# Kernel tuning notes

Hardware: AMD Instinct MI355X
Metric: run time of the kernel (lower is better)

## Reference

```python
import jax, jax.numpy as jnp
import numpy as np

LN_EPS = 1e-5

def _layernorm(x, w, b):
    mu = jnp.mean(x, axis=-1, keepdims=True)
    var = jnp.mean(jnp.square(x - mu), axis=-1, keepdims=True)
    return (x - mu) * jax.lax.rsqrt(var + LN_EPS) * w + b

def setup_inputs() -> dict:
    key = jax.random.key(0)
    ks = jax.random.split(key, 8)
    B, T, C, N = 4, 4096, 1024, 64
    H = 4 * C  # mlp hidden
    x = jax.random.normal(ks[0], (B, T, C), dtype=jnp.float32)
    log_tau = jnp.zeros((N,), dtype=jnp.float32)           # log(1.0)
    log_dt = jnp.zeros((), dtype=jnp.float32)              # log(1.0)
    mix = jax.random.normal(ks[1], (C, N), dtype=jnp.float32) * 0.02
    D = jnp.ones((C,), dtype=jnp.float32)
    norm1_w = jnp.ones((C,), dtype=jnp.float32)
    norm1_b = jnp.zeros((C,), dtype=jnp.float32)
    norm2_w = jnp.ones((C,), dtype=jnp.float32)
    norm2_b = jnp.zeros((C,), dtype=jnp.float32)
    fc1_w = jax.random.normal(ks[2], (H, C), dtype=jnp.float32) * 0.02
    fc1_b = jnp.zeros((H,), dtype=jnp.float32)
    fc2_w = jax.random.normal(ks[3], (C, H), dtype=jnp.float32) * 0.02
    fc2_b = jnp.zeros((C,), dtype=jnp.float32)
    return {"x": x, "log_tau": log_tau, "log_dt": log_dt, "mix": mix, "D": D,
            "norm1_w": norm1_w, "norm1_b": norm1_b, "norm2_w": norm2_w, "norm2_b": norm2_b,
            "fc1_w": fc1_w, "fc1_b": fc1_b, "fc2_w": fc2_w, "fc2_b": fc2_b}

def _s4d(u, log_tau, log_dt, mix, D):
    # u: (B, C, T). K_c[t] = sum_j mix[c,j] * exp(-softplus(log_tau[j])*softplus(log_dt)*t)
    B, C, T = u.shape
    tau = jax.nn.softplus(log_tau)                    # (N,)
    dt = jax.nn.softplus(log_dt)                      # scalar
    t = jnp.arange(T, dtype=jnp.float32)              # (T,)
    E = jnp.exp(-(tau * dt)[:, None] * t[None, :])    # (N, T)
    # torch module computes the exponent table under no_grad (cached buffer)
    E = jax.lax.stop_gradient(E)
    K = mix @ E                                       # (C, T)
    # causal depthwise conv via FFT: y[b,c,t] = sum_{s<=t} K[c,t-s] u[b,c,s]
    n = 2 * T
    Uf = jnp.fft.rfft(u, n=n, axis=-1)                # (B, C, n//2+1)
    Kf = jnp.fft.rfft(K, n=n, axis=-1)                # (C, n//2+1)
    y = jnp.fft.irfft(Uf * Kf[None], n=n, axis=-1)[..., :T]
    return y + D[None, :, None] * u

def reference(x, log_tau, log_dt, mix, D, norm1_w, norm1_b, norm2_w, norm2_b,
              fc1_w, fc1_b, fc2_w, fc2_b):
    # x: (B, T, C)
    h = _layernorm(x, norm1_w, norm1_b)
    h2 = _s4d(jnp.swapaxes(h, 1, 2), log_tau, log_dt, mix, D)  # (B, C, T)
    x = x + jnp.swapaxes(h2, 1, 2)                    # alpha_s4 = 1.0
    g = _layernorm(x, norm2_w, norm2_b)
    g = jax.nn.gelu(g @ fc1_w.T + fc1_b, approximate=False)
    g = g @ fc2_w.T + fc2_b
    return x + g                                      # alpha_mlp = 1.0
```

## Files before the change

kernel.cpp:

```cpp
#include <hip/hip_runtime.h>
#include <math.h>

typedef __attribute__((ext_vector_type(8))) short bf16x8;
typedef __attribute__((ext_vector_type(4))) float f32x4;

__device__ __forceinline__ unsigned short f2bf(float f) {
  union { float f; unsigned u; } v; v.f = f;
  unsigned r = v.u + 0x7fff + ((v.u >> 16) & 1);
  return (unsigned short)(r >> 16);
}

__device__ __forceinline__ float bf2f(unsigned short h) {
  union { unsigned u; float f; } v; v.u = ((unsigned)h) << 16;
  return v.f;
}

__device__ __forceinline__ void gll16(const void* g, void* l) {
  __builtin_amdgcn_global_load_lds(
      (const __attribute__((address_space(1))) void*)g,
      (__attribute__((address_space(3))) void*)l, 16, 0, 0);
}

#define BB 4
#define TT 4096
#define CC 1024
#define HH 4096
#define MM 16384

#define SWZ(row, byteoff) (((row) << 7) + ((byteoff) ^ (((row) & 7) << 4)))

__global__ __launch_bounds__(256) void ln_f32_kernel(
    const float* __restrict__ x, const float* __restrict__ w,
    const float* __restrict__ b, float* __restrict__ out)
{
  size_t row = blockIdx.x;
  const float4* xr = (const float4*)(x + row * CC);
  int tid = threadIdx.x;
  float4 v = xr[tid];
  float s = v.x + v.y + v.z + v.w;
  float sq = v.x*v.x + v.y*v.y + v.z*v.z + v.w*v.w;
  for (int o = 32; o; o >>= 1) { s += __shfl_xor(s, o); sq += __shfl_xor(sq, o); }
  __shared__ float ss[4], ssq[4];
  int wv = tid >> 6, lane = tid & 63;
  if (lane == 0) { ss[wv] = s; ssq[wv] = sq; }
  __syncthreads();
  s = ss[0] + ss[1] + ss[2] + ss[3];
  sq = ssq[0] + ssq[1] + ssq[2] + ssq[3];
  float mu = s * (1.f / CC);
  float var = sq * (1.f / CC) - mu * mu;
  float rstd = rsqrtf(var + 1e-5f);
  float4 wv4 = ((const float4*)w)[tid];
  float4 bv4 = ((const float4*)b)[tid];
  float4 o;
  o.x = (v.x - mu) * rstd * wv4.x + bv4.x;
  o.y = (v.y - mu) * rstd * wv4.y + bv4.y;
  o.z = (v.z - mu) * rstd * wv4.z + bv4.z;
  o.w = (v.w - mu) * rstd * wv4.w + bv4.w;
  ((float4*)(out + row * CC))[tid] = o;
}

__global__ __launch_bounds__(256) void ln_bf16_kernel(
    const float* __restrict__ x, const float* __restrict__ w,
    const float* __restrict__ b, unsigned short* __restrict__ out)
{
  size_t row = blockIdx.x;
  const float4* xr = (const float4*)(x + row * CC);
  int tid = threadIdx.x;
  float4 v = xr[tid];
  float s = v.x + v.y + v.z + v.w;
  float sq = v.x*v.x + v.y*v.y + v.z*v.z + v.w*v.w;
  for (int o = 32; o; o >>= 1) { s += __shfl_xor(s, o); sq += __shfl_xor(sq, o); }
  __shared__ float ss[4], ssq[4];
  int wv = tid >> 6, lane = tid & 63;
  if (lane == 0) { ss[wv] = s; ssq[wv] = sq; }
  __syncthreads();
  s = ss[0] + ss[1] + ss[2] + ss[3];
  sq = ssq[0] + ssq[1] + ssq[2] + ssq[3];
  float mu = s * (1.f / CC);
  float var = sq * (1.f / CC) - mu * mu;
  float rstd = rsqrtf(var + 1e-5f);
  float4 wv4 = ((const float4*)w)[tid];
  float4 bv4 = ((const float4*)b)[tid];
  ushort4 o;
  o.x = f2bf((v.x - mu) * rstd * wv4.x + bv4.x);
  o.y = f2bf((v.y - mu) * rstd * wv4.y + bv4.y);
  o.z = f2bf((v.z - mu) * rstd * wv4.z + bv4.z);
  o.w = f2bf((v.w - mu) * rstd * wv4.w + bv4.w);
  ((ushort4*)(out + row * CC))[tid] = o;
}

__global__ __launch_bounds__(256) void transpose_kernel(
    const float* __restrict__ in, float* __restrict__ out)
{
  __shared__ float tile[64][65];
  size_t boff = (size_t)blockIdx.z * TT * CC;
  int r0 = blockIdx.y * 64;
  int c0 = blockIdx.x * 64;
  int tid = threadIdx.x;
#pragma unroll
  for (int i = 0; i < 16; ++i) {
    int idx = tid + i * 256;
    int r = idx >> 6, cx = idx & 63;
    tile[r][cx] = in[boff + (size_t)(r0 + r) * CC + c0 + cx];
  }
  __syncthreads();
#pragma unroll
  for (int i = 0; i < 16; ++i) {
    int idx = tid + i * 256;
    int r = idx >> 6, cx = idx & 63;
    out[boff + (size_t)(c0 + r) * TT + r0 + cx] = tile[cx][r];
  }
}

__global__ __launch_bounds__(256) void transadd_kernel(
    const float* __restrict__ y, const float* __restrict__ x,
    float* __restrict__ x2)
{
  __shared__ float tile[64][65];
  size_t boff = (size_t)blockIdx.z * TT * CC;
  int t0 = blockIdx.x * 64;
  int c0 = blockIdx.y * 64;
  int tid = threadIdx.x;
#pragma unroll
  for (int i = 0; i < 16; ++i) {
    int idx = tid + i * 256;
    int r = idx >> 6, cx = idx & 63;
    tile[r][cx] = y[boff + (size_t)(c0 + r) * TT + t0 + cx];
  }
  __syncthreads();
#pragma unroll
  for (int i = 0; i < 16; ++i) {
    int idx = tid + i * 256;
    int r = idx >> 6, cx = idx & 63;
    size_t off = boff + (size_t)(t0 + r) * CC + c0 + cx;
    x2[off] = x[off] + tile[cx][r];
  }
}

__global__ __launch_bounds__(256) void s4d_kernel(
    const float* __restrict__ hT,
    const float* __restrict__ log_tau,
    const float* __restrict__ log_dt,
    const float* __restrict__ mix,
    const float* __restrict__ Dv,
    float* __restrict__ y)
{
  int bc = blockIdx.x;
  int c = bc & (CC - 1);
  int tid = threadIdx.x;
  int lane = tid & 63, w = tid >> 6;
  int m = lane & 15, g = lane >> 4;

  __shared__ unsigned short s_uh[64 * 64], s_ul[64 * 64];
  __shared__ unsigned short s_A2[64 * 64], s_Ac[64 * 64];
  __shared__ unsigned short s_T[64 * 64], s_Wt[64 * 64];
  __shared__ float s_P[64 * 64];
  __shared__ float s_a[64], s_rL[64], s_mix[64], s_K[64], s_Kp[4 * 64];

  const float4* urow = (const float4*)(hT + (size_t)bc * TT);
#pragma unroll
  for (int q = 0; q < 4; ++q) {
    int i = tid + q * 256;
    float4 v = urow[i];
    int row = i >> 4;
    int colb = (i & 15) * 8;
    float f[4] = {v.x, v.y, v.z, v.w};
    ushort4 hh, ll;
    unsigned short* hp = (unsigned short*)&hh;
    unsigned short* lp = (unsigned short*)&ll;
#pragma unroll
    for (int r = 0; r < 4; ++r) {
      unsigned short hb = f2bf(f[r]);
      hp[r] = hb;
      lp[r] = f2bf(f[r] - bf2f(hb));
    }
    *(ushort4*)((char*)s_uh + SWZ(row, colb)) = hh;
    *(ushort4*)((char*)s_ul + SWZ(row, colb)) = ll;
  }
  if (tid < 64) {
    float lt = log_tau[tid];
    float tau = (lt > 20.f) ? lt : log1pf(expf(lt));
    float ld = log_dt[0];
    float dt = (ld > 20.f) ? ld : log1pf(expf(ld));
    float a = tau * dt;
    s_a[tid] = a;
    s_rL[tid] = expf(-64.f * a);
    s_mix[tid] = mix[c * 64 + tid];
  }
  __syncthreads();

#pragma unroll
  for (int e = 0; e < 16; ++e) {
    int idx = tid + e * 256;
    int rA = idx >> 6, cA = idx & 63;
    s_A2[SWZ(rA, cA * 2) >> 1] = f2bf(expf(-s_a[rA] * (float)(63 - cA)));
    s_Ac[SWZ(rA, cA * 2) >> 1] = f2bf(expf(-s_a[cA] * (float)(rA + 1)));
  }
  __syncthreads();

  {
    int d = tid & 63, q = tid >> 6;
    float p = 0.f;
    if (d == 0) {
#pragma unroll
      for (int j = 16 * q; j < 16 * q + 16; ++j) p += s_mix[j];
    } else {
#pragma unroll
      for (int j = 16 * q; j < 16 * q + 16; ++j)
        p = fmaf(s_mix[j], bf2f(s_Ac[SWZ(d - 1, j * 2) >> 1]), p);
    }
    s_Kp[q * 64 + d] = p;
  }

  {
    f32x4 accP[4] = {};
    bf16x8 a2f[2];
#pragma unroll
    for (int ks = 0; ks < 2; ++ks)
      a2f[ks] = *(const bf16x8*)((const char*)s_A2 + SWZ(16 * w + m, ks * 64 + g * 16));
#pragma unroll
    for (int ct = 0; ct < 4; ++ct) {
#pragma unroll
      for (int ks = 0; ks < 2; ++ks) {
        bf16x8 bh = *(const bf16x8*)((const char*)s_uh + SWZ(ct * 16 + m, ks * 64 + g * 16));
        bf16x8 bl = *(const bf16x8*)((const char*)s_ul + SWZ(ct * 16 + m, ks * 64 + g * 16));
        accP[ct] = __builtin_amdgcn_mfma_f32_16x16x32_bf16(a2f[ks], bh, accP[ct], 0, 0, 0);
        accP[ct] = __builtin_amdgcn_mfma_f32_16x16x32_bf16(a2f[ks], bl, accP[ct], 0, 0, 0);
      }
    }
#pragma unroll
    for (int ct = 0; ct < 4; ++ct)
      *(f32x4*)&s_P[(ct * 16 + m) * 64 + 16 * w + g * 4] = accP[ct];
  }
  __syncthreads();

  if (tid < 64)
    s_K[tid] = s_Kp[tid] + s_Kp[64 + tid] + s_Kp[128 + tid] + s_Kp[192 + tid];
  __syncthreads();

#pragma unroll
  for (int e = 0; e < 16; ++e) {
    int idx = tid + e * 256;
    int t = idx >> 6, s = idx & 63;
    float val = (s <= t) ? s_K[t - s] : 0.f;
    s_T[SWZ(t, s * 2) >> 1] = f2bf(val);
  }
  if (tid < 64) {
    int j = tid;
    float S = 0.f, rL = s_rL[j], mj = s_mix[j];
    for (int k = 0; k < 64; ++k) {
      s_Wt[SWZ(k, j * 2) >> 1] = f2bf(mj * S);
      S = fmaf(rL, S, s_P[k * 64 + j]);
    }
  }
  __syncthreads();

  f32x4 accY[4] = {};
  {
    bf16x8 acf[2], tf[2];
#pragma unroll
    for (int ks = 0; ks < 2; ++ks) {
      acf[ks] = *(const bf16x8*)((const char*)s_Ac + SWZ(16 * w + m, ks * 64 + g * 16));
      tf[ks]  = *(const bf16x8*)((const char*)s_T  + SWZ(16 * w + m, ks * 64 + g * 16));
    }
#pragma unroll
    for (int ct = 0; ct < 4; ++ct) {
#pragma unroll
      for (int ks = 0; ks < 2; ++ks) {
        bf16x8 bw  = *(const bf16x8*)((const char*)s_Wt + SWZ(ct * 16 + m, ks * 64 + g * 16));
        bf16x8 uhf = *(const bf16x8*)((const char*)s_uh + SWZ(ct * 16 + m, ks * 64 + g * 16));
        bf16x8 ulf = *(const bf16x8*)((const char*)s_ul + SWZ(ct * 16 + m, ks * 64 + g * 16));
        accY[ct] = __builtin_amdgcn_mfma_f32_16x16x32_bf16(acf[ks], bw,  accY[ct], 0, 0, 0);
        accY[ct] = __builtin_amdgcn_mfma_f32_16x16x32_bf16(tf[ks],  uhf, accY[ct], 0, 0, 0);
        accY[ct] = __builtin_amdgcn_mfma_f32_16x16x32_bf16(tf[ks],  ulf, accY[ct], 0, 0, 0);
      }
    }
  }

  float Dc = Dv[c];
  float* yrow = y + (size_t)bc * TT;
#pragma unroll
  for (int ct = 0; ct < 4; ++ct) {
    int k = ct * 16 + m;
    int t0 = 16 * w + g * 4;
    float4 o;
    float* op = (float*)&o;
#pragma unroll
    for (int r = 0; r < 4; ++r) {
      int t = t0 + r;
      float uf = bf2f(s_uh[SWZ(k, t * 2) >> 1]) + bf2f(s_ul[SWZ(k, t * 2) >> 1]);
      op[r] = accY[ct][r] + Dc * uf;
    }
    *(float4*)(yrow + k * 64 + t0) = o;
  }
}

__global__ __launch_bounds__(256) void cvt_bf16_kernel(
    const float* __restrict__ in, unsigned short* __restrict__ out)
{
  int i = blockIdx.x * 256 + threadIdx.x;
  float4 v = ((const float4*)in)[i];
  ushort4 o;
  o.x = f2bf(v.x); o.y = f2bf(v.y); o.z = f2bf(v.z); o.w = f2bf(v.w);
  ((ushort4*)out)[i] = o;
}


#define GEMM256_BODY(A_, lda_, B_, ldb_, K_)                                   \
  __shared__ unsigned short sA[2][256 * 64];                                   \
  __shared__ unsigned short sB[2][256 * 64];                                   \
  int id = blockIdx.x;                                                         \
  int swz = (id & 7) * cpx + (id >> 3);                                        \
  int m0 = (swz / NB) * 256, n0 = (swz % NB) * 256;                            \
  int tid = threadIdx.x, lane = tid & 63;                                      \
  int wid = tid >> 6, wm = wid >> 2, wn = wid & 3;                             \
  int m = lane & 15, g = lane >> 4;                                            \
  const unsigned short* aSrc[4];                                               \
  const unsigned short* bSrc[4];                                               \
  int ldsOff[4];                                                               \
  _Pragma("unroll")                                                            \
  for (int i = 0; i < 4; ++i) {                                                \
    int j = i * 512 + tid;                                                     \
    int row = j >> 3;                                                          \
    int colb = ((j & 7) * 16) ^ ((row & 7) << 4);                              \
    aSrc[i] = (A_) + (size_t)(m0 + row) * (lda_) + (colb >> 1);                \
    bSrc[i] = (B_) + (size_t)(n0 + row) * (ldb_) + (colb >> 1);                \
    ldsOff[i] = j * 8;                                                         \
  }                                                                            \
  f32x4 acc[8][4] = {};                                                        \
  int nt = (K_) >> 6;                                                          \
                                                \
  _Pragma("unroll")                                                            \
  for (int i = 0; i < 4; ++i) gll16(aSrc[i], &sA[0][ldsOff[i]]);               \
  _Pragma("unroll")                                                            \
  for (int i = 0; i < 4; ++i) gll16(bSrc[i], &sB[0][ldsOff[i]]);               \
  _Pragma("unroll")                                                            \
  for (int i = 0; i < 4; ++i) gll16(aSrc[i] + 64, &sA[1][ldsOff[i]]);          \
  _Pragma("unroll")                                                            \
  for (int i = 0; i < 4; ++i) gll16(bSrc[i] + 64, &sB[1][ldsOff[i]]);          \
  asm volatile("s_waitcnt vmcnt(8)" ::: "memory");                             \
  asm volatile("s_barrier" ::: "memory");                                      \
  int cur = 0;                                                                 \
  for (int kt = 0; kt < nt; ++kt) {                                            \
    const unsigned short* sAc = sA[cur];                                       \
    const unsigned short* sBc = sB[cur];                                       \
    bf16x8 bfr[4][2];                                                          \
    _Pragma("unroll")                                                          \
    for (int ni = 0; ni < 4; ++ni)                                             \
      _Pragma("unroll")                                                        \
      for (int ks = 0; ks < 2; ++ks)                                           \
        bfr[ni][ks] = *(const bf16x8*)((const char*)sBc +                      \
                        SWZ(wn * 64 + ni * 16 + m, ks * 64 + g * 16));         \
    _Pragma("unroll")                                                          \
    for (int q = 0; q < 4; ++q) {                                              \
      bf16x8 af[2][2];                                                         \
      _Pragma("unroll")                                                        \
      for (int mi = 0; mi < 2; ++mi)                                           \
        _Pragma("unroll")                                                      \
        for (int ks = 0; ks < 2; ++ks)                                         \
          af[mi][ks] = *(const bf16x8*)((const char*)sAc +                     \
                         SWZ(wm * 128 + (q * 2 + mi) * 16 + m,                 \
                             ks * 64 + g * 16));                               \
      __builtin_amdgcn_s_setprio(1);                                           \
      _Pragma("unroll")                                                        \
      for (int mi = 0; mi < 2; ++mi)                                           \
        _Pragma("unroll")                                                      \
        for (int ni = 0; ni < 4; ++ni) {                                       \
          acc[q * 2 + mi][ni] = __builtin_amdgcn_mfma_f32_16x16x32_bf16(       \
              af[mi][0], bfr[ni][0], acc[q * 2 + mi][ni], 0, 0, 0);            \
          acc[q * 2 + mi][ni] = __builtin_amdgcn_mfma_f32_16x16x32_bf16(       \
              af[mi][1], bfr[ni][1], acc[q * 2 + mi][ni], 0, 0, 0);            \
        }                                                                      \
      __builtin_amdgcn_s_setprio(0);                                           \
    }                                                                          \
    if (kt + 1 < nt) {                                                         \
      asm volatile("s_barrier" ::: "memory");   \
      if (kt + 2 < nt) {                                                       \
        int ko = (kt + 2) << 6;                                                \
        _Pragma("unroll")                                                      \
        for (int i = 0; i < 4; ++i) gll16(aSrc[i] + ko, &sA[cur][ldsOff[i]]);  \
        _Pragma("unroll")                                                      \
        for (int i = 0; i < 4; ++i) gll16(bSrc[i] + ko, &sB[cur][ldsOff[i]]);  \
        asm volatile("s_waitcnt vmcnt(8)" ::: "memory");                       \
      } else {                                                                 \
        asm volatile("s_waitcnt vmcnt(0)" ::: "memory");                       \
      }                                                                        \
      asm volatile("s_barrier" ::: "memory");   \
      cur ^= 1;                                                                \
    }                                                                          \
  }

__global__ __launch_bounds__(512, 2) void gemm_gelu_kernel(
    const unsigned short* __restrict__ A, int lda,
    const unsigned short* __restrict__ Bw, int ldb,
    const float* __restrict__ bias, unsigned short* __restrict__ Out, int ldo,
    int K, int NB, int cpx)
{
  GEMM256_BODY(A, lda, Bw, ldb, K)

#pragma unroll
  for (int mi = 0; mi < 8; ++mi) {
    int row = m0 + wm * 128 + mi * 16 + g * 4;
#pragma unroll
    for (int ni = 0; ni < 4; ++ni) {
      int col = n0 + wn * 64 + ni * 16 + m;
      float bcol = bias[col];
#pragma unroll
      for (int r = 0; r < 4; ++r) {
        float v = acc[mi][ni][r] + bcol;
        v = 0.5f * v * (1.f + erff(v * 0.70710678118f));
        Out[(size_t)(row + r) * ldo + col] = f2bf(v);
      }
    }
  }
}

__global__ __launch_bounds__(512, 2) void gemm_acc_kernel(
    const unsigned short* __restrict__ A, int lda,
    const unsigned short* __restrict__ Bw, int ldb,
    const float* __restrict__ bias,
    const float* add, float* Out, int K, int NB, int cpx)
{
  GEMM256_BODY(A, lda, Bw, ldb, K)

#pragma unroll
  for (int mi = 0; mi < 8; ++mi) {
    int row = m0 + wm * 128 + mi * 16 + g * 4;
#pragma unroll
    for (int ni = 0; ni < 4; ++ni) {
      int col = n0 + wn * 64 + ni * 16 + m;
      float bcol = bias ? bias[col] : 0.f;
#pragma unroll
      for (int r = 0; r < 4; ++r) {
        size_t off = (size_t)(row + r) * CC + col;
        Out[off] = acc[mi][ni][r] + bcol + add[off];
      }
    }
  }
}

extern "C" void kernel_launch(void* const* d_in, const int* in_sizes, int n_in,
                              void* d_out, int out_size, void* d_ws, size_t ws_size,
                              hipStream_t stream)
{
  const float* x       = (const float*)d_in[0];
  const float* log_tau = (const float*)d_in[1];
  const float* log_dt  = (const float*)d_in[2];
  const float* mix     = (const float*)d_in[3];
  const float* Dv      = (const float*)d_in[4];
  const float* n1w     = (const float*)d_in[5];
  const float* n1b     = (const float*)d_in[6];
  const float* n2w     = (const float*)d_in[7];
  const float* n2b     = (const float*)d_in[8];
  const float* w1      = (const float*)d_in[9];
  const float* b1      = (const float*)d_in[10];
  const float* w2      = (const float*)d_in[11];
  const float* b2      = (const float*)d_in[12];

  char* ws = (char*)d_ws;
  float* buf0 = (float*)ws;
  float* buf1 = (float*)(ws + (64ull << 20));
  unsigned short* a2  = (unsigned short*)(ws + (128ull << 20));
  unsigned short* w1b = (unsigned short*)(ws + (160ull << 20));
  unsigned short* w2b = (unsigned short*)(ws + (168ull << 20));
  unsigned short* act = (unsigned short*)buf0;
  float* out = (float*)d_out;

  ln_f32_kernel<<<MM, 256, 0, stream>>>(x, n1w, n1b, buf0);
  transpose_kernel<<<dim3(CC / 64, TT / 64, BB), 256, 0, stream>>>(buf0, buf1);
  s4d_kernel<<<BB * CC, 256, 0, stream>>>(buf1, log_tau, log_dt, mix, Dv, buf0);
  transadd_kernel<<<dim3(TT / 64, CC / 64, BB), 256, 0, stream>>>(buf0, x, buf1);
  ln_bf16_kernel<<<MM, 256, 0, stream>>>(buf1, n2w, n2b, a2);
  cvt_bf16_kernel<<<(HH * CC / 4) / 256, 256, 0, stream>>>(w1, w1b);
  cvt_bf16_kernel<<<(HH * CC / 4) / 256, 256, 0, stream>>>(w2, w2b);

  gemm_gelu_kernel<<<512, 512, 0, stream>>>(
      a2, CC, w1b, CC, b1, act, 2048, CC, 8, 64);
  gemm_acc_kernel<<<256, 512, 0, stream>>>(
      act, 2048, w2b, HH, b2, buf1, out, 2048, 4, 32);
  gemm_gelu_kernel<<<512, 512, 0, stream>>>(
      a2, CC, w1b + (size_t)2048 * CC, CC, b1 + 2048, act, 2048, CC, 8, 64);
  gemm_acc_kernel<<<256, 512, 0, stream>>>(
      act, 2048, w2b + 2048, HH, (const float*)nullptr, out, out, 2048, 4, 32);
}
```

Measured before the change: 747.0 us.

## Interleave GEMM tile loads across four compute phases per K-step

Restructures the 256x256 bf16 MFMA GEMM main loop into four compute phases separated by barriers. The next-next K tile's global-to-LDS loads are split across those phases instead of issued in one burst at the end of the iteration. Load rows are remapped so each phase's slice of the buffer is already free when its reload is issued. The aim is to spread memory traffic evenly and overlap it with MFMA work. The cost is more barriers per K-step and more delicate vmcnt accounting.

```diff
diff --git a/kernel.cpp b/kernel.cpp
--- a/kernel.cpp
+++ b/kernel.cpp
@@ -306,7 +306,26 @@
 }
 
 
-#define GEMM256_BODY(A_, lda_, B_, ldb_, K_)                                   \
+#define PHASE_COMPUTE(q)                                                       \
+  {                                                                            \
+    bf16x8 af[2][2];                                                           \
+    _Pragma("unroll") for (int mi = 0; mi < 2; ++mi)                           \
+      _Pragma("unroll") for (int ks = 0; ks < 2; ++ks)                         \
+        af[mi][ks] = *(const bf16x8*)((const char*)sAc +                       \
+                       SWZ(wm * 128 + (q) * 32 + mi * 16 + m,                  \
+                           ks * 64 + g * 16));                                 \
+    __builtin_amdgcn_s_setprio(1);                                             \
+    _Pragma("unroll") for (int mi = 0; mi < 2; ++mi)                           \
+      _Pragma("unroll") for (int ni = 0; ni < 4; ++ni) {                       \
+        acc[(q) * 2 + mi][ni] = __builtin_amdgcn_mfma_f32_16x16x32_bf16(       \
+            af[mi][0], bfr[ni][0], acc[(q) * 2 + mi][ni], 0, 0, 0);            \
+        acc[(q) * 2 + mi][ni] = __builtin_amdgcn_mfma_f32_16x16x32_bf16(       \
+            af[mi][1], bfr[ni][1], acc[(q) * 2 + mi][ni], 0, 0, 0);            \
+      }                                                                        \
+    __builtin_amdgcn_s_setprio(0);                                             \
+  }
+
+#define GEMM256_8PH(A_, lda_, B_, ldb_, K_)                                    \
   __shared__ unsigned short sA[2][256 * 64];                                   \
   __shared__ unsigned short sB[2][256 * 64];                                   \
   int id = blockIdx.x;                                                         \
@@ -315,79 +334,78 @@
   int tid = threadIdx.x, lane = tid & 63;                                      \
   int wid = tid >> 6, wm = wid >> 2, wn = wid & 3;                             \
   int m = lane & 15, g = lane >> 4;                                            \
+  int r5 = tid >> 3;                                                \
+  int ce = ((((tid & 7) * 16) ^ ((r5 & 7) << 4)) >> 1);  \
+  int lde = (tid & 7) * 8;                           \
+  int rowA[4], rowB[4];                                                        \
+  _Pragma("unroll") for (int q = 0; q < 4; ++q) {                              \
+    rowA[q] = (r5 < 32) ? (q * 32 + r5) : (96 + q * 32 + r5);                  \
+    rowB[q] = q * 64 + r5;                                                     \
+  }                                                                            \
   const unsigned short* aSrc[4];                                               \
   const unsigned short* bSrc[4];                                               \
-  int ldsOff[4];                                                               \
-  _Pragma("unroll")                                                            \
-  for (int i = 0; i < 4; ++i) {                                                \
-    int j = i * 512 + tid;                                                     \
-    int row = j >> 3;                                                          \
-    int colb = ((j & 7) * 16) ^ ((row & 7) << 4);                              \
-    aSrc[i] = (A_) + (size_t)(m0 + row) * (lda_) + (colb >> 1);                \
-    bSrc[i] = (B_) + (size_t)(n0 + row) * (ldb_) + (colb >> 1);                \
-    ldsOff[i] = j * 8;                                                         \
+  int aOff[4], bOff[4];                                                        \
+  _Pragma("unroll") for (int q = 0; q < 4; ++q) {                              \
+    aSrc[q] = (A_) + (size_t)(m0 + rowA[q]) * (lda_) + ce;                     \
+    bSrc[q] = (B_) + (size_t)(n0 + rowB[q]) * (ldb_) + ce;                     \
+    aOff[q] = rowA[q] * 64 + lde;                                              \
+    bOff[q] = rowB[q] * 64 + lde;                                              \
   }                                                                            \
   f32x4 acc[8][4] = {};                                                        \
   int nt = (K_) >> 6;                                                          \
-                                                \
-  _Pragma("unroll")                                                            \
-  for (int i = 0; i < 4; ++i) gll16(aSrc[i], &sA[0][ldsOff[i]]);               \
-  _Pragma("unroll")                                                            \
-  for (int i = 0; i < 4; ++i) gll16(bSrc[i], &sB[0][ldsOff[i]]);               \
-  _Pragma("unroll")                                                            \
-  for (int i = 0; i < 4; ++i) gll16(aSrc[i] + 64, &sA[1][ldsOff[i]]);          \
-  _Pragma("unroll")                                                            \
-  for (int i = 0; i < 4; ++i) gll16(bSrc[i] + 64, &sB[1][ldsOff[i]]);          \
-  asm volatile("s_waitcnt vmcnt(8)" ::: "memory");                             \
-  asm volatile("s_barrier" ::: "memory");                                      \
-  int cur = 0;                                                                 \
+        \
+  _Pragma("unroll") for (int q = 0; q < 4; ++q) {                              \
+    gll16(bSrc[q], &sB[0][bOff[q]]);                                           \
+    gll16(aSrc[q], &sA[0][aOff[q]]);                                           \
+  }                                                                            \
+  _Pragma("unroll") for (int q = 0; q < 4; ++q)                                \
+    gll16(bSrc[q] + 64, &sB[1][bOff[q]]);                                      \
+  _Pragma("unroll") for (int q = 0; q < 3; ++q)                                \
+    gll16(aSrc[q] + 64, &sA[1][aOff[q]]);                                      \
   for (int kt = 0; kt < nt; ++kt) {                                            \
+    int cur = kt & 1;                                                          \
     const unsigned short* sAc = sA[cur];                                       \
     const unsigned short* sBc = sB[cur];                                       \
+          \
+    if (kt + 1 < nt) {                                                         \
+      asm volatile("s_waitcnt vmcnt(7)" ::: "memory");                         \
+      gll16(aSrc[3] + (kt + 1) * 64, &sA[cur ^ 1][aOff[3]]);                   \
+    } else {                                                                   \
+      asm volatile("s_waitcnt vmcnt(0)" ::: "memory");                         \
+    }                                                                          \
+    asm volatile("s_barrier" ::: "memory");                                    \
     bf16x8 bfr[4][2];                                                          \
-    _Pragma("unroll")                                                          \
-    for (int ni = 0; ni < 4; ++ni)                                             \
-      _Pragma("unroll")                                                        \
-      for (int ks = 0; ks < 2; ++ks)                                           \
+    _Pragma("unroll") for (int ni = 0; ni < 4; ++ni)                           \
+      _Pragma("unroll") for (int ks = 0; ks < 2; ++ks)                         \
         bfr[ni][ks] = *(const bf16x8*)((const char*)sBc +                      \
                         SWZ(wn * 64 + ni * 16 + m, ks * 64 + g * 16));         \
-    _Pragma("unroll")                                                          \
-    for (int q = 0; q < 4; ++q) {                                              \
-      bf16x8 af[2][2];                                                         \
-      _Pragma("unroll")                                                        \
-      for (int mi = 0; mi < 2; ++mi)                                           \
-        _Pragma("unroll")                                                      \
-        for (int ks = 0; ks < 2; ++ks)                                         \
-          af[mi][ks] = *(const bf16x8*)((const char*)sAc +                     \
-                         SWZ(wm * 128 + (q * 2 + mi) * 16 + m,                 \
-                             ks * 64 + g * 16));                               \
-      __builtin_amdgcn_s_setprio(1);                                           \
-      _Pragma("unroll")                                                        \
-      for (int mi = 0; mi < 2; ++mi)                                           \
-        _Pragma("unroll")                                                      \
-        for (int ni = 0; ni < 4; ++ni) {                                       \
-          acc[q * 2 + mi][ni] = __builtin_amdgcn_mfma_f32_16x16x32_bf16(       \
-              af[mi][0], bfr[ni][0], acc[q * 2 + mi][ni], 0, 0, 0);            \
-          acc[q * 2 + mi][ni] = __builtin_amdgcn_mfma_f32_16x16x32_bf16(       \
-              af[mi][1], bfr[ni][1], acc[q * 2 + mi][ni], 0, 0, 0);            \
-        }                                                                      \
-      __builtin_amdgcn_s_setprio(0);                                           \
+    PHASE_COMPUTE(0)                                                           \
+    asm volatile("s_barrier" ::: "memory");                                    \
+                       \
+    if (kt + 2 < nt) {                                                         \
+      int ko = (kt + 2) * 64;                                                  \
+      gll16(bSrc[0] + ko, &sB[cur][bOff[0]]);                                  \
+      gll16(bSrc[1] + ko, &sB[cur][bOff[1]]);                                  \
     }                                                                          \
-    if (kt + 1 < nt) {                                                         \
-      asm volatile("s_barrier" ::: "memory");   \
-      if (kt + 2 < nt) {                                                       \
-        int ko = (kt + 2) << 6;                                                \
-        _Pragma("unroll")                                                      \
-        for (int i = 0; i < 4; ++i) gll16(aSrc[i] + ko, &sA[cur][ldsOff[i]]);  \
-        _Pragma("unroll")                                                      \
-        for (int i = 0; i < 4; ++i) gll16(bSrc[i] + ko, &sB[cur][ldsOff[i]]);  \
-        asm volatile("s_waitcnt vmcnt(8)" ::: "memory");                       \
-      } else {                                                                 \
-        asm volatile("s_waitcnt vmcnt(0)" ::: "memory");                       \
-      }                                                                        \
-      asm volatile("s_barrier" ::: "memory");   \
-      cur ^= 1;                                                                \
+    PHASE_COMPUTE(1)                                                           \
+    asm volatile("s_barrier" ::: "memory");                                    \
+                    \
+    if (kt + 2 < nt) {                                                         \
+      int ko = (kt + 2) * 64;                                                  \
+      gll16(bSrc[2] + ko, &sB[cur][bOff[2]]);                                  \
+      gll16(bSrc[3] + ko, &sB[cur][bOff[3]]);                                  \
+      gll16(aSrc[0] + ko, &sA[cur][aOff[0]]);                                  \
     }                                                                          \
+    PHASE_COMPUTE(2)                                                           \
+    asm volatile("s_barrier" ::: "memory");                                    \
+               \
+    if (kt + 2 < nt) {                                                         \
+      int ko = (kt + 2) * 64;                                                  \
+      gll16(aSrc[1] + ko, &sA[cur][aOff[1]]);                                  \
+      gll16(aSrc[2] + ko, &sA[cur][aOff[2]]);                                  \
+    }                                                                          \
+    PHASE_COMPUTE(3)                                                           \
+    asm volatile("s_barrier" ::: "memory");                                    \
   }
 
 __global__ __launch_bounds__(512, 2) void gemm_gelu_kernel(
@@ -396,7 +414,7 @@
     const float* __restrict__ bias, unsigned short* __restrict__ Out, int ldo,
     int K, int NB, int cpx)
 {
-  GEMM256_BODY(A, lda, Bw, ldb, K)
+  GEMM256_8PH(A, lda, Bw, ldb, K)
 
 #pragma unroll
   for (int mi = 0; mi < 8; ++mi) {
@@ -421,7 +439,7 @@
     const float* __restrict__ bias,
     const float* add, float* Out, int K, int NB, int cpx)
 {
-  GEMM256_BODY(A, lda, Bw, ldb, K)
+  GEMM256_8PH(A, lda, Bw, ldb, K)
 
 #pragma unroll
   for (int mi = 0; mi < 8; ++mi) {
```

Result: faster. 732.1 us (-2.0%).
